# Kernel optimization log

Measured on AMD Instinct MI355X. Metric: run time of the kernel, lower is better.

Reference implementation:

```python
import jax, jax.numpy as jnp
import numpy as np
from jax import lax

T = 16        # in_length
E = 32        # input_embedding_size_d
H = 64        # encoder_size
NG = 32       # vehicles per scene group
G = 1024      # number of scene groups
N = G * NG    # total vehicles
C = 3         # class_num

leaky = lambda x: jax.nn.leaky_relu(x, 0.1)

def _gru_final(x_seq, Wih, Whh, bih, bhh):
    # x_seq: (T, N, E). PyTorch GRU gate order: r, z, n. Returns final hidden (N, H).
    def step(h, x):
        gx = x @ Wih.T + bih
        gh = h @ Whh.T + bhh
        xr, xz, xn = jnp.split(gx, 3, axis=-1)
        hr, hz, hn = jnp.split(gh, 3, axis=-1)
        r = jax.nn.sigmoid(xr + hr)
        z = jax.nn.sigmoid(xz + hz)
        ng = jnp.tanh(xn + r * hn)
        return (1.0 - z) * ng + z * h, None
    h0 = jnp.zeros((x_seq.shape[1], Whh.shape[1]), x_seq.dtype)
    hT, _ = lax.scan(step, h0, x_seq)
    return hT

def setup_inputs() -> dict:
    key = jax.random.key(0)
    ks = jax.random.split(key, 24)
    def rn(k, shape, fan):
        return jax.random.normal(k, shape, jnp.float32) * np.float32(1.0 / np.sqrt(fan))
    inp = {}
    inp["scene"] = jax.random.normal(ks[0], (N, 2 * T), jnp.float32)
    inp["condition"] = jax.random.randint(ks[1], (N,), 0, C, jnp.int32)
    inp["hero_pos_index"] = jax.random.randint(ks[2], (G,), 0, N, jnp.int32)
    inp["nbrs_pos_index"] = jax.random.randint(ks[3], (N,), 0, N, jnp.int32)
    inp["index_div"] = jnp.arange(N, dtype=jnp.int32).reshape(G, NG)
    # ip_emb_d: Linear(2, E)
    inp["W_emb"] = rn(ks[4], (2, E), 2)
    inp["b_emb"] = jnp.zeros((E,), jnp.float32)
    # forward / backward GRUs (weight_ih: (3H,E), weight_hh: (3H,H))
    inp["Wih_f"] = rn(ks[5], (3 * H, E), E); inp["Whh_f"] = rn(ks[6], (3 * H, H), H)
    inp["bih_f"] = jnp.zeros((3 * H,), jnp.float32); inp["bhh_f"] = jnp.zeros((3 * H,), jnp.float32)
    inp["Wih_b"] = rn(ks[7], (3 * H, E), E); inp["Whh_b"] = rn(ks[8], (3 * H, H), H)
    inp["bih_b"] = jnp.zeros((3 * H,), jnp.float32); inp["bhh_b"] = jnp.zeros((3 * H,), jnp.float32)
    # mlp: Linear(H, H//2)
    inp["Wm"] = rn(ks[9], (H, H // 2), H); inp["bm"] = jnp.zeros((H // 2,), jnp.float32)
    # spatial_mlp: Linear(2T, H) -> Linear(H, H//2)
    inp["Ws1"] = rn(ks[10], (2 * T, H), 2 * T); inp["bs1"] = jnp.zeros((H,), jnp.float32)
    inp["Ws2"] = rn(ks[11], (H, H // 2), H); inp["bs2"] = jnp.zeros((H // 2,), jnp.float32)
    # op_d: Linear(H, H//4) -> Linear(H//4, C)
    inp["Wo1"] = rn(ks[12], (H, H // 4), H); inp["bo1"] = jnp.zeros((H // 4,), jnp.float32)
    inp["Wo2"] = rn(ks[13], (H // 4, C), H // 4); inp["bo2"] = jnp.zeros((C,), jnp.float32)
    return inp

def reference(scene, condition, hero_pos_index, nbrs_pos_index, index_div,
              W_emb, b_emb, Wih_f, Whh_f, bih_f, bhh_f, Wih_b, Whh_b, bih_b, bhh_b,
              Wm, bm, Ws1, bs1, Ws2, bs2, Wo1, bo1, Wo2, bo2):
    n_total = scene.shape[0]
    # scene.view(-1,2,T).permute(2,0,1) -> (T, N, 2)
    scene_t = scene.reshape(n_total, 2, T).transpose(2, 0, 1)
    emb = leaky(scene_t @ W_emb + b_emb)                 # (T, N, E)
    h_f = _gru_final(emb, Wih_f, Whh_f, bih_f, bhh_f)    # (N, H)
    h_b = _gru_final(emb[::-1], Wih_b, Whh_b, bih_b, bhh_b)
    seq_enc = leaky(((h_f + h_b) * 0.5) @ Wm + bm)       # (N, H//2)
    # pairwise relative features within each group: rel[g, j, i] = x_i - x_j
    feat_g = scene[index_div]                            # (G, n, 2T); row layout == permute(1,2,0).view(-1,2T)
    rel = feat_g[:, None, :, :] - feat_g[:, :, None, :]  # (G, n, n, 2T)
    enc = leaky(leaky(rel @ Ws1 + bs1) @ Ws2 + bs2)      # (G, n, n, H//2)
    # diagonal pairs (i==j) are dropped in the original; subtract mlp(0) then divide by n-1
    zero_enc = leaky(leaky(bs1) @ Ws2 + bs2)             # (H//2,)
    n_grp = index_div.shape[1]
    pooled = (enc.sum(axis=2) - zero_enc) / (n_grp - 1)  # (G, n, H//2)
    pooled = pooled.reshape(n_total, -1)                 # group-concat order == vehicle order (arange groups)
    full_enc = jnp.concatenate([seq_enc, pooled], axis=1)  # (N, H)
    x_logit = leaky(full_enc @ Wo1 + bo1) @ Wo2 + bo2      # (N, C)
    return x_logit, full_enc
```

## Files before the change

kernel.cpp:

```cpp
#include <hip/hip_runtime.h>
#include <hip/hip_bf16.h>

#define TT 16
#define EE 32
#define HH 64
#define NGRP 32
#define CC 3

typedef __attribute__((ext_vector_type(8))) short short8;
typedef __attribute__((ext_vector_type(4))) float floatx4;

#define MFMA16(a, b, c) __builtin_amdgcn_mfma_f32_16x16x32_bf16((a), (b), (c), 0, 0, 0)

#define RLN2 1.4426950408889634f

__device__ __forceinline__ float leakyf(float x) { return fmaxf(x, 0.1f * x); }
__device__ __forceinline__ short f2bf(float x) {
    unsigned u = __float_as_uint(x);
    return (short)((u + 0x7FFFu + ((u >> 16) & 1u)) >> 16);
}
__device__ __forceinline__ short f2bf_h(float x) {
    return (short)((__float_as_uint(x) + 0x8000u) >> 16);
}
__device__ __forceinline__ float bf2f(short s) {
    return __uint_as_float(((unsigned)(unsigned short)s) << 16);
}
__device__ __forceinline__ short8 ld8bf(const float* __restrict__ p) {
    const float4 a = *(const float4*)p;
    const float4 b = *(const float4*)(p + 4);
    short8 v;
    v[0] = f2bf(a.x); v[1] = f2bf(a.y); v[2] = f2bf(a.z); v[3] = f2bf(a.w);
    v[4] = f2bf(b.x); v[5] = f2bf(b.y); v[6] = f2bf(b.z); v[7] = f2bf(b.w);
    return v;
}
__device__ __forceinline__ short8 ld8bfs(const float* __restrict__ p, float s) {
    const float4 a = *(const float4*)p;
    const float4 b = *(const float4*)(p + 4);
    short8 v;
    v[0] = f2bf(a.x * s); v[1] = f2bf(a.y * s); v[2] = f2bf(a.z * s); v[3] = f2bf(a.w * s);
    v[4] = f2bf(b.x * s); v[5] = f2bf(b.y * s); v[6] = f2bf(b.z * s); v[7] = f2bf(b.w * s);
    return v;
}

__global__ __launch_bounds__(512, 4) void fused_kernel(
    const float* __restrict__ scene, const int* __restrict__ index_div,
    const float* __restrict__ W_emb, const float* __restrict__ b_emb,
    const float* __restrict__ Wih_f, const float* __restrict__ Whh_f,
    const float* __restrict__ bih_f, const float* __restrict__ bhh_f,
    const float* __restrict__ Wih_b, const float* __restrict__ Whh_b,
    const float* __restrict__ bih_b, const float* __restrict__ bhh_b,
    const float* __restrict__ Wm, const float* __restrict__ bm,
    const float* __restrict__ Ws1, const float* __restrict__ bs1,
    const float* __restrict__ Ws2, const float* __restrict__ bs2,
    const float* __restrict__ Wo1, const float* __restrict__ bo1,
    const float* __restrict__ Wo2, const float* __restrict__ bo2,
    float* __restrict__ full_enc, float* __restrict__ out)
{
    __shared__ float sscene[32][33];
    __shared__ __align__(16) union SmemU {
        struct {
            short Xall[16 * 2 * 64 * 8];
            short Hf[2 * 2 * 2 * 2 * 64 * 8];
        } g;
        struct {
            float su[NGRP][68];
            float fe[NGRP][68];
            float swo1[1024];
            float szero[32];
        } s;
    } sm;

    const int g    = blockIdx.x;
    const int tid  = threadIdx.x;
    const int lane = tid & 63;
    const int w    = __builtin_amdgcn_readfirstlane(tid >> 6);
    const int dir  = w >> 2;
    const int wd   = w & 3;
    const int cc   = lane & 15;
    const int quad = lane >> 4;
    const int j    = wd * 16 + cc;
    const int ks_w = j >> 5;
    const int qa_w = (j >> 3) & 3;
    const int ii_w = j & 7;
    const int rlane = (lane & 48) | ((lane & 3) << 2) | ((lane >> 2) & 3);

    #pragma unroll
    for (int rep = 0; rep < 2; ++rep) {
        const int idx = tid + rep * 512;
        const int v = idx >> 5, c = idx & 31;
        const int n = index_div[g * NGRP + v];
        sscene[c][v] = scene[n * 32 + c];
    }

    const float* Wih = dir ? Wih_b : Wih_f;
    const float* Whh = dir ? Whh_b : Whh_f;
    const float* bih = dir ? bih_b : bih_f;
    const float* bhh = dir ? bhh_b : bhh_f;
    const int k0 = quad * 8;
    const float SRZ = -RLN2, SN = 2.0f * RLN2;
    const short8 Br0  = ld8bfs(Whh + (j      ) * 64 + k0,      SRZ);
    const short8 Br1  = ld8bfs(Whh + (j      ) * 64 + 32 + k0, SRZ);
    const short8 Br2  = ld8bfs(Wih + (j      ) * 32 + k0,      SRZ);
    const short8 Bz0  = ld8bfs(Whh + (j +  64) * 64 + k0,      SRZ);
    const short8 Bz1  = ld8bfs(Whh + (j +  64) * 64 + 32 + k0, SRZ);
    const short8 Bz2  = ld8bfs(Wih + (j +  64) * 32 + k0,      SRZ);
    const short8 Bhn0 = ld8bfs(Whh + (j + 128) * 64 + k0,      SN);
    const short8 Bhn1 = ld8bfs(Whh + (j + 128) * 64 + 32 + k0, SN);
    const short8 Bxn  = ld8bfs(Wih + (j + 128) * 32 + k0,      SN);
    const float vb_r  = SRZ * (bih[j] + bhh[j]);
    const float vb_z  = SRZ * (bih[j + 64] + bhh[j + 64]);
    const float vb_xn = SN * bih[j + 128];
    const float vb_hn = SN * bhh[j + 128];

    __syncthreads();

    {
        const int t   = tid >> 5;
        const int veh = tid & 31;
        const float xs = sscene[t][veh];
        const float ys = sscene[16 + t][veh];
        const int mt = veh >> 4;
        const int m  = veh & 15;
        #pragma unroll
        for (int q = 0; q < 4; ++q) {
            short8 v;
            #pragma unroll
            for (int i2 = 0; i2 < 8; ++i2) {
                const int e = q * 8 + i2;
                v[i2] = f2bf(leakyf(fmaf(xs, W_emb[e], fmaf(ys, W_emb[EE + e], b_emb[e]))));
            }
            *(short8*)&sm.g.Xall[(((t * 2 + mt) * 64) + q * 16 + m) * 8] = v;
        }
        const short8 z8 = {0, 0, 0, 0, 0, 0, 0, 0};
        *(short8*)&sm.g.Hf[(tid >> 8) * 4096 + (tid & 255) * 8] = z8;
    }

    float h_reg[8];
    #pragma unroll
    for (int i = 0; i < 8; ++i) h_reg[i] = 0.0f;

    const int hf_dir = dir * 4096;
    __syncthreads();

    #pragma unroll 2
    for (int s = 0; s < TT; ++s) {
        const int pb = s & 1, nb = pb ^ 1;
        const int t  = dir ? (TT - 1 - s) : s;
        const short* HfD = &sm.g.Hf[hf_dir + pb * 2048];
        short*       HfN = &sm.g.Hf[hf_dir + nb * 2048];
        #pragma unroll
        for (int mt = 0; mt < 2; ++mt) {
            const short8 Ah0 = *(const short8*)&HfD[((0 * 2 + mt) * 64 + rlane) * 8];
            const short8 Ah1 = *(const short8*)&HfD[((1 * 2 + mt) * 64 + rlane) * 8];
            const short8 Axx = *(const short8*)&sm.g.Xall[((t * 2 + mt) * 64 + lane) * 8];
            const floatx4 z4 = {0.f, 0.f, 0.f, 0.f};
            const floatx4 ar  = MFMA16(Axx, Br2, MFMA16(Ah1, Br1, MFMA16(Ah0, Br0, z4)));
            const floatx4 az  = MFMA16(Axx, Bz2, MFMA16(Ah1, Bz1, MFMA16(Ah0, Bz0, z4)));
            const floatx4 ahn = MFMA16(Ah1, Bhn1, MFMA16(Ah0, Bhn0, z4));
            const floatx4 axn = MFMA16(Axx, Bxn, z4);
            #pragma unroll
            for (int r = 0; r < 4; ++r) {
                const float rr = __builtin_amdgcn_rcpf(1.0f + __builtin_amdgcn_exp2f(ar[r] + vb_r));
                const float zz = __builtin_amdgcn_rcpf(1.0f + __builtin_amdgcn_exp2f(az[r] + vb_z));
                const float y  = fmaf(rr, ahn[r] + vb_hn, axn[r] + vb_xn);
                const float ng = fmaf(-2.0f,
                                      __builtin_amdgcn_rcpf(__builtin_amdgcn_exp2f(y) + 1.0f),
                                      1.0f);
                const float h0 = h_reg[mt * 4 + r];
                h_reg[mt * 4 + r] = fmaf(zz, h0 - ng, ng);
            }
        }
        #pragma unroll
        for (int mt = 0; mt < 2; ++mt) {
            #pragma unroll
            for (int r = 0; r < 4; ++r) {
                const int slot = qa_w * 16 + r * 4 + quad;
                HfN[((ks_w * 2 + mt) * 64 + slot) * 8 + ii_w] = f2bf_h(h_reg[mt * 4 + r]);
            }
        }
        __syncthreads();
    }

    if (w < 4) {
        const int nt   = w >> 1;
        const int mt_e = w & 1;
        const int n_col = nt * 16 + cc;
        short8 Bm0, Bm1;
        #pragma unroll
        for (int i = 0; i < 8; ++i) {
            Bm0[i] = f2bf(Wm[(     quad * 8 + i) * 32 + n_col]);
            Bm1[i] = f2bf(Wm[(32 + quad * 8 + i) * 32 + n_col]);
        }
        short8 A0, A1;
        #pragma unroll
        for (int ks = 0; ks < 2; ++ks) {
            const short8 F = *(const short8*)&sm.g.Hf[0    + ((ks * 2 + mt_e) * 64 + rlane) * 8];
            const short8 B = *(const short8*)&sm.g.Hf[4096 + ((ks * 2 + mt_e) * 64 + rlane) * 8];
            #pragma unroll
            for (int i = 0; i < 8; ++i) {
                const short v = f2bf(0.5f * (bf2f(F[i]) + bf2f(B[i])));
                if (ks == 0) A0[i] = v; else A1[i] = v;
            }
        }
        const floatx4 z4 = {0.f, 0.f, 0.f, 0.f};
        const floatx4 acc = MFMA16(A1, Bm1, MFMA16(A0, Bm0, z4));
        const float bmn = bm[n_col];
        #pragma unroll
        for (int r = 0; r < 4; ++r) {
            const int veh = mt_e * 16 + quad * 4 + r;
            const float sv = leakyf(acc[r] + bmn);
            const int n = index_div[g * NGRP + veh];
            full_enc[n * HH + n_col] = sv;
            sm.s.fe[veh][n_col] = sv;
        }
    } else {
        const int l  = tid & 255;
        const int v  = l >> 3;
        const int d0 = (l & 7) * 8;
        float acc[8];
        #pragma unroll
        for (int i = 0; i < 8; ++i) acc[i] = 0.0f;
        #pragma unroll
        for (int e = 0; e < EE; ++e) {
            const float f = sscene[e][v];
            const float4 w0 = *(const float4*)&Ws1[e * 64 + d0];
            const float4 w1 = *(const float4*)&Ws1[e * 64 + d0 + 4];
            acc[0] = fmaf(f, w0.x, acc[0]); acc[1] = fmaf(f, w0.y, acc[1]);
            acc[2] = fmaf(f, w0.z, acc[2]); acc[3] = fmaf(f, w0.w, acc[3]);
            acc[4] = fmaf(f, w1.x, acc[4]); acc[5] = fmaf(f, w1.y, acc[5]);
            acc[6] = fmaf(f, w1.z, acc[6]); acc[7] = fmaf(f, w1.w, acc[7]);
        }
        #pragma unroll
        for (int i = 0; i < 8; ++i) sm.s.su[v][d0 + i] = acc[i];
        *(float4*)&sm.s.swo1[l * 4] = *(const float4*)&Wo1[l * 4];
        if (l < 32) {
            float zs = bs2[l];
            #pragma unroll
            for (int d = 0; d < HH; ++d) zs = fmaf(leakyf(bs1[d]), Ws2[d * 32 + l], zs);
            sm.s.szero[l] = leakyf(zs);
        }
    }

    short8 Bw00, Bw01, Bw10, Bw11;
    #pragma unroll
    for (int i = 0; i < 8; ++i) {
        Bw00[i] = f2bf(Ws2[(     quad * 8 + i) * 32 + cc]);
        Bw01[i] = f2bf(Ws2[(32 + quad * 8 + i) * 32 + cc]);
        Bw10[i] = f2bf(Ws2[(     quad * 8 + i) * 32 + 16 + cc]);
        Bw11[i] = f2bf(Ws2[(32 + quad * 8 + i) * 32 + 16 + cc]);
    }
    float bsq0[8], bsq1[8];
    #pragma unroll
    for (int i = 0; i < 8; ++i) {
        bsq0[i] = bs1[quad * 8 + i];
        bsq1[i] = bs1[32 + quad * 8 + i];
    }
    const float bs2c0 = bs2[cc], bs2c1 = bs2[16 + cc];
    __syncthreads();

    #pragma unroll 2
    for (int jj = 0; jj < 4; ++jj) {
        const int jrow = w * 4 + jj;
        float vj0[8], vj1[8];
        #pragma unroll
        for (int i = 0; i < 8; ++i) {
            vj0[i] = sm.s.su[jrow][quad * 8 + i] - bsq0[i];
            vj1[i] = sm.s.su[jrow][32 + quad * 8 + i] - bsq1[i];
        }
        float acc0 = 0.0f, acc1 = 0.0f;
        #pragma unroll
        for (int it = 0; it < 2; ++it) {
            const int irow = it * 16 + cc;
            const float4 p0 = *(const float4*)&sm.s.su[irow][quad * 8];
            const float4 p1 = *(const float4*)&sm.s.su[irow][quad * 8 + 4];
            const float4 p2 = *(const float4*)&sm.s.su[irow][32 + quad * 8];
            const float4 p3 = *(const float4*)&sm.s.su[irow][32 + quad * 8 + 4];
            short8 A0, A1;
            A0[0] = f2bf(leakyf(p0.x - vj0[0])); A0[1] = f2bf(leakyf(p0.y - vj0[1]));
            A0[2] = f2bf(leakyf(p0.z - vj0[2])); A0[3] = f2bf(leakyf(p0.w - vj0[3]));
            A0[4] = f2bf(leakyf(p1.x - vj0[4])); A0[5] = f2bf(leakyf(p1.y - vj0[5]));
            A0[6] = f2bf(leakyf(p1.z - vj0[6])); A0[7] = f2bf(leakyf(p1.w - vj0[7]));
            A1[0] = f2bf(leakyf(p2.x - vj1[0])); A1[1] = f2bf(leakyf(p2.y - vj1[1]));
            A1[2] = f2bf(leakyf(p2.z - vj1[2])); A1[3] = f2bf(leakyf(p2.w - vj1[3]));
            A1[4] = f2bf(leakyf(p3.x - vj1[4])); A1[5] = f2bf(leakyf(p3.y - vj1[5]));
            A1[6] = f2bf(leakyf(p3.z - vj1[6])); A1[7] = f2bf(leakyf(p3.w - vj1[7]));
            const floatx4 z4 = {0.f, 0.f, 0.f, 0.f};
            const floatx4 D0 = MFMA16(A1, Bw01, MFMA16(A0, Bw00, z4));
            const floatx4 D1 = MFMA16(A1, Bw11, MFMA16(A0, Bw10, z4));
            #pragma unroll
            for (int r = 0; r < 4; ++r) {
                acc0 += leakyf(D0[r] + bs2c0);
                acc1 += leakyf(D1[r] + bs2c1);
            }
        }
        acc0 += __shfl_xor(acc0, 16, 64); acc0 += __shfl_xor(acc0, 32, 64);
        acc1 += __shfl_xor(acc1, 16, 64); acc1 += __shfl_xor(acc1, 32, 64);
        const int n = index_div[g * NGRP + jrow];
        if (quad == 0) {
            const float pv = (acc0 - sm.s.szero[cc]) * (1.0f / 31.0f);
            full_enc[n * HH + 32 + cc] = pv;
            sm.s.fe[jrow][32 + cc] = pv;
        } else if (quad == 1) {
            const float pv = (acc1 - sm.s.szero[16 + cc]) * (1.0f / 31.0f);
            full_enc[n * HH + 48 + cc] = pv;
            sm.s.fe[jrow][48 + cc] = pv;
        }
    }
    __syncthreads();

    {
        const int veh = tid >> 4;
        const int p   = tid & 15;
        float a = bo1[p];
        #pragma unroll
        for (int k = 0; k < HH; ++k)
            a = fmaf(sm.s.fe[veh][k], sm.s.swo1[k * 16 + p], a);
        a = leakyf(a);
        float l0 = a * Wo2[p * 3 + 0];
        float l1 = a * Wo2[p * 3 + 1];
        float l2 = a * Wo2[p * 3 + 2];
        #pragma unroll
        for (int off = 1; off < 16; off <<= 1) {
            l0 += __shfl_xor(l0, off, 64);
            l1 += __shfl_xor(l1, off, 64);
            l2 += __shfl_xor(l2, off, 64);
        }
        if (p == 0) {
            const int n = index_div[g * NGRP + veh];
            out[n * 3 + 0] = l0 + bo2[0];
            out[n * 3 + 1] = l1 + bo2[1];
            out[n * 3 + 2] = l2 + bo2[2];
        }
    }
}

extern "C" void kernel_launch(void* const* d_in, const int* in_sizes, int n_in,
                              void* d_out, int out_size, void* d_ws, size_t ws_size,
                              hipStream_t stream) {
    const float* scene     = (const float*)d_in[0];
    const int*   index_div = (const int*)d_in[4];
    const float* W_emb = (const float*)d_in[5];
    const float* b_emb = (const float*)d_in[6];
    const float* Wih_f = (const float*)d_in[7];
    const float* Whh_f = (const float*)d_in[8];
    const float* bih_f = (const float*)d_in[9];
    const float* bhh_f = (const float*)d_in[10];
    const float* Wih_b = (const float*)d_in[11];
    const float* Whh_b = (const float*)d_in[12];
    const float* bih_b = (const float*)d_in[13];
    const float* bhh_b = (const float*)d_in[14];
    const float* Wm  = (const float*)d_in[15];
    const float* bm  = (const float*)d_in[16];
    const float* Ws1 = (const float*)d_in[17];
    const float* bs1 = (const float*)d_in[18];
    const float* Ws2 = (const float*)d_in[19];
    const float* bs2 = (const float*)d_in[20];
    const float* Wo1 = (const float*)d_in[21];
    const float* bo1 = (const float*)d_in[22];
    const float* Wo2 = (const float*)d_in[23];
    const float* bo2 = (const float*)d_in[24];

    const int N = in_sizes[0] / (2 * TT);
    const int G = in_sizes[4] / NGRP;

    float* out      = (float*)d_out;
    float* full_enc = out + (size_t)N * CC;

    fused_kernel<<<dim3(G), dim3(512), 0, stream>>>(
        scene, index_div, W_emb, b_emb, Wih_f, Whh_f, bih_f, bhh_f,
        Wih_b, Whh_b, bih_b, bhh_b, Wm, bm, Ws1, bs1, Ws2, bs2,
        Wo1, bo1, Wo2, bo2, full_enc, out);
}
```

Measured before the change: 193.0 us.

## Compute GRU input embeddings per step into double buffer to shrink LDS

Instead of precomputing bf16 embeddings for all 16 timesteps into a large LDS array, each step computes the next timestep's embedding into a small double-buffered slot. Wo1 staging is moved into the reused sscene region, and the union is rearranged so Hf survives into the spatial phase. The goal is less shared memory per block, allowing more resident blocks and better latency hiding, at the cost of extra ALU work inside the serial recurrence loop. Embedding rounding also switches to the cheaper round-half-up conversion.

```diff
diff --git a/kernel.cpp b/kernel.cpp
--- a/kernel.cpp
+++ b/kernel.cpp
@@ -8,6 +8,7 @@
 #define CC 3
 
 typedef __attribute__((ext_vector_type(8))) short short8;
+typedef __attribute__((ext_vector_type(4))) short short4v;
 typedef __attribute__((ext_vector_type(4))) float floatx4;
 
 #define MFMA16(a, b, c) __builtin_amdgcn_mfma_f32_16x16x32_bf16((a), (b), (c), 0, 0, 0)
@@ -59,13 +60,13 @@
     __shared__ float sscene[32][33];
     __shared__ __align__(16) union SmemU {
         struct {
-            short Xall[16 * 2 * 64 * 8];
             short Hf[2 * 2 * 2 * 2 * 64 * 8];
+            short Xb[2 * 2 * 2 * 64 * 8];
         } g;
         struct {
+            short Hf_keep[2 * 2 * 2 * 2 * 64 * 8];
             float su[NGRP][68];
             float fe[NGRP][68];
-            float swo1[1024];
             float szero[32];
         } s;
     } sm;
@@ -112,27 +113,33 @@
     const float vb_xn = SN * bih[j + 128];
     const float vb_hn = SN * bhh[j + 128];
 
+    const int l     = tid & 255;
+    const int veh_x = l & 31;
+    const int q2    = l >> 5;
+    const int e0    = q2 * 4;
+    float w0e[4], w1e[4], bbe[4];
+    #pragma unroll
+    for (int d = 0; d < 4; ++d) {
+        w0e[d] = W_emb[e0 + d];
+        w1e[d] = W_emb[EE + e0 + d];
+        bbe[d] = b_emb[e0 + d];
+    }
+    const int xoff = dir * 2048 + ((veh_x >> 4) * 64 + (q2 >> 1) * 16 + (veh_x & 15)) * 8
+                   + (q2 & 1) * 4;
+
     __syncthreads();
 
     {
-        const int t   = tid >> 5;
-        const int veh = tid & 31;
-        const float xs = sscene[t][veh];
-        const float ys = sscene[16 + t][veh];
-        const int mt = veh >> 4;
-        const int m  = veh & 15;
-        #pragma unroll
-        for (int q = 0; q < 4; ++q) {
-            short8 v;
-            #pragma unroll
-            for (int i2 = 0; i2 < 8; ++i2) {
-                const int e = q * 8 + i2;
-                v[i2] = f2bf(leakyf(fmaf(xs, W_emb[e], fmaf(ys, W_emb[EE + e], b_emb[e]))));
-            }
-            *(short8*)&sm.g.Xall[(((t * 2 + mt) * 64) + q * 16 + m) * 8] = v;
-        }
         const short8 z8 = {0, 0, 0, 0, 0, 0, 0, 0};
         *(short8*)&sm.g.Hf[(tid >> 8) * 4096 + (tid & 255) * 8] = z8;
+        const int t0 = dir ? (TT - 1) : 0;
+        const float xs = sscene[t0][veh_x];
+        const float ys = sscene[16 + t0][veh_x];
+        short4v v;
+        #pragma unroll
+        for (int d = 0; d < 4; ++d)
+            v[d] = f2bf_h(leakyf(fmaf(xs, w0e[d], fmaf(ys, w1e[d], bbe[d]))));
+        *(short4v*)&sm.g.Xb[xoff] = v;
     }
 
     float h_reg[8];
@@ -145,14 +152,14 @@
     #pragma unroll 2
     for (int s = 0; s < TT; ++s) {
         const int pb = s & 1, nb = pb ^ 1;
-        const int t  = dir ? (TT - 1 - s) : s;
         const short* HfD = &sm.g.Hf[hf_dir + pb * 2048];
         short*       HfN = &sm.g.Hf[hf_dir + nb * 2048];
+        const short* XbD = &sm.g.Xb[dir * 2048 + pb * 1024];
         #pragma unroll
         for (int mt = 0; mt < 2; ++mt) {
             const short8 Ah0 = *(const short8*)&HfD[((0 * 2 + mt) * 64 + rlane) * 8];
             const short8 Ah1 = *(const short8*)&HfD[((1 * 2 + mt) * 64 + rlane) * 8];
-            const short8 Axx = *(const short8*)&sm.g.Xall[((t * 2 + mt) * 64 + lane) * 8];
+            const short8 Axx = *(const short8*)&XbD[(mt * 64 + lane) * 8];
             const floatx4 z4 = {0.f, 0.f, 0.f, 0.f};
             const floatx4 ar  = MFMA16(Axx, Br2, MFMA16(Ah1, Br1, MFMA16(Ah0, Br0, z4)));
             const floatx4 az  = MFMA16(Axx, Bz2, MFMA16(Ah1, Bz1, MFMA16(Ah0, Bz0, z4)));
@@ -178,6 +185,16 @@
                 HfN[((ks_w * 2 + mt) * 64 + slot) * 8 + ii_w] = f2bf_h(h_reg[mt * 4 + r]);
             }
         }
+        if (s + 1 < TT) {
+            const int tn = dir ? (TT - 2 - s) : (s + 1);
+            const float xs = sscene[tn][veh_x];
+            const float ys = sscene[16 + tn][veh_x];
+            short4v v;
+            #pragma unroll
+            for (int d = 0; d < 4; ++d)
+                v[d] = f2bf_h(leakyf(fmaf(xs, w0e[d], fmaf(ys, w1e[d], bbe[d]))));
+            *(short4v*)&sm.g.Xb[xoff + nb * 1024] = v;
+        }
         __syncthreads();
     }
 
@@ -214,7 +231,6 @@
             sm.s.fe[veh][n_col] = sv;
         }
     } else {
-        const int l  = tid & 255;
         const int v  = l >> 3;
         const int d0 = (l & 7) * 8;
         float acc[8];
@@ -232,7 +248,6 @@
         }
         #pragma unroll
         for (int i = 0; i < 8; ++i) sm.s.su[v][d0 + i] = acc[i];
-        *(float4*)&sm.s.swo1[l * 4] = *(const float4*)&Wo1[l * 4];
         if (l < 32) {
             float zs = bs2[l];
             #pragma unroll
@@ -257,6 +272,9 @@
     }
     const float bs2c0 = bs2[cc], bs2c1 = bs2[16 + cc];
     __syncthreads();
+
+    float* swo1 = (float*)&sscene[0][0];
+    *(float2*)&swo1[tid * 2] = *(const float2*)&Wo1[tid * 2];
 
     #pragma unroll 2
     for (int jj = 0; jj < 4; ++jj) {
@@ -314,7 +332,7 @@
         float a = bo1[p];
         #pragma unroll
         for (int k = 0; k < HH; ++k)
-            a = fmaf(sm.s.fe[veh][k], sm.s.swo1[k * 16 + p], a);
+            a = fmaf(sm.s.fe[veh][k], swo1[k * 16 + p], a);
         a = leakyf(a);
         float l0 = a * Wo2[p * 3 + 0];
         float l1 = a * Wo2[p * 3 + 1];
```

After: 195.4 us. About the same (+1.3%).
